# Kernel optimization log

Measured on AMD Instinct MI355X. Metric: run time of the kernel, lower is better.

Reference implementation:

```python
import jax, jax.numpy as jnp
import numpy as np

N, C, HD, E, T, HS, WS = 8, 256, 8, 64, 16, 14, 14
S = HS * WS
EPS = 1e-5
FACTOR = 1.0 / np.sqrt(S * E).astype(np.float32)


def hswish(x):
    return x * jnp.clip(x + 3.0, 0.0, 6.0) * (1.0 / 6.0)


def _bn(x, g, b, m, v):
    shp = (1, -1, 1, 1, 1)
    scale = g / jnp.sqrt(v + EPS)
    return (x - m.reshape(shp)) * scale.reshape(shp) + b.reshape(shp)


def _dwconv(x, w):
    # depthwise Conv3d kernel (1,3,3), padding (0,1,1), groups=C
    return jax.lax.conv_general_dilated(
        x, w, window_strides=(1, 1, 1),
        padding=((0, 0), (1, 1), (1, 1)),
        dimension_numbers=('NCDHW', 'OIDHW', 'NCDHW'),
        feature_group_count=x.shape[1])


def _project(x, dw, g1, b1, m1, v1, pw, pb=None, bn2=None):
    h = hswish(_bn(_dwconv(x, dw), g1, b1, m1, v1))
    y = jnp.einsum('ncthw,oc->nothw', h, pw)
    if pb is not None:
        y = y + pb.reshape(1, -1, 1, 1, 1)
    if bn2 is not None:
        y = _bn(y, *bn2)
    return y


def setup_inputs() -> dict:
    key = jax.random.key(0)
    ks = jax.random.split(key, 8)
    d = {}
    d['x'] = jax.random.normal(ks[0], (N, C, T, HS, WS), jnp.float32)
    for name, k, out in (('theta', ks[1], HD * E), ('phi', ks[2], HD * E), ('g', ks[3], HD * C)):
        k1, k2 = jax.random.split(k)
        d[name + '_dw'] = jax.random.normal(k1, (C, 1, 1, 3, 3), jnp.float32) * 0.2
        d[name + '_bn1_g'] = jnp.ones((C,), jnp.float32)
        d[name + '_bn1_b'] = jnp.zeros((C,), jnp.float32)
        d[name + '_bn1_m'] = jnp.zeros((C,), jnp.float32)
        d[name + '_bn1_v'] = jnp.ones((C,), jnp.float32)
        d[name + '_pw'] = jax.random.normal(k2, (out, C), jnp.float32) * (1.0 / np.sqrt(C).astype(np.float32))
    d['theta_pb'] = jnp.zeros((HD * E,), jnp.float32)
    d['phi_pb'] = jnp.zeros((HD * E,), jnp.float32)
    d['g_bn2_g'] = jnp.ones((HD * C,), jnp.float32)
    d['g_bn2_b'] = jnp.zeros((HD * C,), jnp.float32)
    d['g_bn2_m'] = jnp.zeros((HD * C,), jnp.float32)
    d['g_bn2_v'] = jnp.ones((HD * C,), jnp.float32)
    d['heads_w'] = jax.random.normal(ks[4], (HD, HD), jnp.float32)
    return d


def reference(x, theta_dw, theta_bn1_g, theta_bn1_b, theta_bn1_m, theta_bn1_v, theta_pw, theta_pb,
              phi_dw, phi_bn1_g, phi_bn1_b, phi_bn1_m, phi_bn1_v, phi_pw, phi_pb,
              g_dw, g_bn1_g, g_bn1_b, g_bn1_m, g_bn1_v, g_pw,
              g_bn2_g, g_bn2_b, g_bn2_m, g_bn2_v, heads_w):
    th = _project(x, theta_dw, theta_bn1_g, theta_bn1_b, theta_bn1_m, theta_bn1_v, theta_pw, pb=theta_pb)
    ph = _project(x, phi_dw, phi_bn1_g, phi_bn1_b, phi_bn1_m, phi_bn1_v, phi_pw, pb=phi_pb)
    gg = hswish(_project(x, g_dw, g_bn1_g, g_bn1_b, g_bn1_m, g_bn1_v, g_pw,
                         bn2=(g_bn2_g, g_bn2_b, g_bn2_m, g_bn2_v)))
    TH = th.reshape(N, HD, E, T, S)   # theta features
    PH = ph.reshape(N, HD, E, T, S)   # phi features
    G5 = gg.reshape(N, HD, C, T, S)   # value features
    # adjacency over temporal nodes: [N,H,T,T]
    adj = jax.nn.softmax(FACTOR * jnp.einsum('nhets,nheus->nhtu', TH, PH), axis=-1)
    # GCN step: [N,H,T,C,S]
    gcn = hswish(jnp.einsum('nhtu,nhcus->nhtcs', adj, G5))
    # head-mix attention: [N,T,H]
    hf = gcn.mean(axis=(3, 4)).transpose(0, 2, 1)
    attn = jax.nn.softmax(hf @ heads_w, axis=-1)
    # combine heads: [N,C,T,S] -> [N,C,T,Hs,Ws]
    z = jnp.einsum('nhtcs,nth->ncts', gcn, attn).reshape(N, C, T, HS, WS)
    return hswish(x + z)
```

## Files before the change

### kernel.cpp

```cpp
#include <hip/hip_runtime.h>
#include <hip/hip_bf16.h>

typedef __hip_bfloat16 bf16;
typedef __attribute__((ext_vector_type(4))) float f32x4;
typedef __attribute__((ext_vector_type(8))) short s16x8;

#define DEV static __device__ __forceinline__

namespace {

constexpr float kEPS = 1e-5f;
constexpr float kFACTOR = 1.0f / 112.0f;

DEV float hswish_f(float v) { return v * fminf(fmaxf(v + 3.f, 0.f), 6.f) * (1.f / 6.f); }

DEV void gload_lds16(const bf16* g, bf16* l) {
  __builtin_amdgcn_global_load_lds(
      (const __attribute__((address_space(1))) unsigned int*)g,
      (__attribute__((address_space(3))) unsigned int*)l, 16, 0, 0);
}

__global__ void cvt_pw_kernel(const float* __restrict__ a,
                              const float* __restrict__ b,
                              const float* __restrict__ cG,
                              const float* __restrict__ g2g, const float* __restrict__ g2b,
                              const float* __restrict__ g2m, const float* __restrict__ g2v,
                              bf16* __restrict__ oa, bf16* __restrict__ ob,
                              bf16* __restrict__ oc, float* __restrict__ bnscl,
                              float* __restrict__ bnsft) {
  int i = blockIdx.x * 256 + threadIdx.x;
  if (i < 512 * 256) {
    oa[i] = __float2bfloat16(a[i]);
    ob[i] = __float2bfloat16(b[i]);
  }
  if (i < 2048 * 256) {
    int r = i >> 8, k = i & 255;
    int h = r >> 8, c = r & 255;
    oc[(c * 8 + h) * 256 + k] = __float2bfloat16(cG[i]);
  }
  if (i < 2048) {
    int c = i >> 3, h = i & 7, ref = h * 256 + c;
    float s = g2g[ref] * rsqrtf(g2v[ref] + kEPS);
    bnscl[i] = s;
    bnsft[i] = g2b[ref] - g2m[ref] * s;
  }
}

__global__ __launch_bounds__(256) void conv_kernel(
    const float* __restrict__ x,
    const float* __restrict__ tdw, const float* __restrict__ tg,
    const float* __restrict__ tb, const float* __restrict__ tm, const float* __restrict__ tv,
    const float* __restrict__ pdw, const float* __restrict__ pg,
    const float* __restrict__ pb, const float* __restrict__ pm, const float* __restrict__ pv,
    const float* __restrict__ gdw, const float* __restrict__ gG,
    const float* __restrict__ gb, const float* __restrict__ gm, const float* __restrict__ gv,
    bf16* __restrict__ h_t, bf16* __restrict__ h_p, bf16* __restrict__ h_g) {
  int bid = blockIdx.x;
  int cb = bid & 3, t = (bid >> 2) & 15, n = bid >> 6;
  int c0 = cb * 64;
  __shared__ float xs[64][197];
  __shared__ float wts[3][64][9];
  __shared__ float sc[3][64], sh[3][64];
  int tid = threadIdx.x;
  for (int i = tid; i < 64 * 9; i += 256) {
    int cl = i / 9, k = i % 9;
    wts[0][cl][k] = tdw[(c0 + cl) * 9 + k];
    wts[1][cl][k] = pdw[(c0 + cl) * 9 + k];
    wts[2][cl][k] = gdw[(c0 + cl) * 9 + k];
  }
  if (tid < 64) {
    int c = c0 + tid;
    float s0 = tg[c] * rsqrtf(tv[c] + kEPS);
    sc[0][tid] = s0; sh[0][tid] = tb[c] - tm[c] * s0;
    float s1 = pg[c] * rsqrtf(pv[c] + kEPS);
    sc[1][tid] = s1; sh[1][tid] = pb[c] - pm[c] * s1;
    float s2 = gG[c] * rsqrtf(gv[c] + kEPS);
    sc[2][tid] = s2; sh[2][tid] = gb[c] - gm[c] * s2;
  }
  const float* xb = x + ((size_t)(n * 256 + c0) * 16 + t) * 196;
  for (int i = tid; i < 64 * 196; i += 256) {
    int cl = i / 196, s = i % 196;
    xs[cl][s] = xb[(size_t)cl * 3136 + s];
  }
  __syncthreads();
  for (int i = tid; i < 64 * 196; i += 256) {
    int cl = i & 63, sp = i >> 6;
    int hs = sp / 14, wsp = sp % 14;
    float a0 = 0.f, a1 = 0.f, a2 = 0.f;
    #pragma unroll
    for (int dy = -1; dy <= 1; ++dy) {
      int yy = hs + dy;
      if (yy < 0 || yy >= 14) continue;
      #pragma unroll
      for (int dx = -1; dx <= 1; ++dx) {
        int xx = wsp + dx;
        if (xx < 0 || xx >= 14) continue;
        float v = xs[cl][yy * 14 + xx];
        int k = (dy + 1) * 3 + (dx + 1);
        a0 = fmaf(wts[0][cl][k], v, a0);
        a1 = fmaf(wts[1][cl][k], v, a1);
        a2 = fmaf(wts[2][cl][k], v, a2);
      }
    }
    a0 = hswish_f(a0 * sc[0][cl] + sh[0][cl]);
    a1 = hswish_f(a1 * sc[1][cl] + sh[1][cl]);
    a2 = hswish_f(a2 * sc[2][cl] + sh[2][cl]);
    size_t oidx = ((size_t)n * 3136 + t * 196 + sp) * 256 + c0 + cl;
    h_t[oidx] = __float2bfloat16(a0);
    h_p[oidx] = __float2bfloat16(a1);
    h_g[oidx] = __float2bfloat16(a2);
  }
}

__global__ __launch_bounds__(256) void gemm_op_kernel(
    const bf16* __restrict__ A,
    const bf16* __restrict__ B,
    bf16* __restrict__ D,
    const float* __restrict__ bias) {
  int mt = blockIdx.x, nt = blockIdx.y, n = blockIdx.z;
  __shared__ __align__(16) bf16 lds_a[128 * 64];
  __shared__ __align__(16) bf16 lds_b[64 * 64];
  int tid = threadIdx.x;
  int wid = tid >> 6, lane = tid & 63;
  int wr = wid >> 1, wc = wid & 1;
  int l15 = lane & 15, lh = lane >> 4;
  f32x4 acc[4][2];
  #pragma unroll
  for (int m = 0; m < 4; ++m)
    #pragma unroll
    for (int q = 0; q < 2; ++q) acc[m][q] = (f32x4){0.f, 0.f, 0.f, 0.f};
  const bf16* Ab = A + (size_t)mt * 128 * 256;
  const bf16* Bb = B + ((size_t)n * 3136 + (size_t)nt * 64) * 256;
  for (int k0 = 0; k0 < 256; k0 += 64) {
    #pragma unroll
    for (int it = 0; it < 4; ++it) {
      int g = tid + it * 256;
      int row = g >> 3, c16 = g & 7;
      int4 v = *(const int4*)(Ab + (size_t)row * 256 + k0 + c16 * 8);
      *(int4*)((char*)lds_a + row * 128 + ((c16 * 16) ^ ((row & 7) << 4))) = v;
    }
    #pragma unroll
    for (int it = 0; it < 2; ++it) {
      int g = tid + it * 256;
      int row = g >> 3, c16 = g & 7;
      int4 v = *(const int4*)(Bb + (size_t)row * 256 + k0 + c16 * 8);
      *(int4*)((char*)lds_b + row * 128 + ((c16 * 16) ^ ((row & 7) << 4))) = v;
    }
    __syncthreads();
    #pragma unroll
    for (int kk = 0; kk < 64; kk += 32) {
      s16x8 af[4], bfr[2];
      #pragma unroll
      for (int m = 0; m < 4; ++m) {
        int row = wr * 64 + m * 16 + l15;
        af[m] = *(const s16x8*)((const char*)lds_a + row * 128 +
                                (((kk + lh * 8) * 2) ^ ((row & 7) << 4)));
      }
      #pragma unroll
      for (int q = 0; q < 2; ++q) {
        int row = wc * 32 + q * 16 + l15;
        bfr[q] = *(const s16x8*)((const char*)lds_b + row * 128 +
                                 (((kk + lh * 8) * 2) ^ ((row & 7) << 4)));
      }
      #pragma unroll
      for (int m = 0; m < 4; ++m)
        #pragma unroll
        for (int q = 0; q < 2; ++q)
          acc[m][q] = __builtin_amdgcn_mfma_f32_16x16x32_bf16(af[m], bfr[q], acc[m][q], 0, 0, 0);
    }
    __syncthreads();
  }
  #pragma unroll
  for (int m = 0; m < 4; ++m) {
    #pragma unroll
    for (int q = 0; q < 2; ++q) {
      int col = wc * 32 + q * 16 + l15;
      #pragma unroll
      for (int r = 0; r < 4; ++r) {
        int row = wr * 64 + m * 16 + lh * 4 + r;
        float v = acc[m][q][r] + bias[mt * 128 + row];
        *(bf16*)((char*)lds_a + row * 128 + ((col * 2) ^ ((row & 7) << 4))) =
            __float2bfloat16(v);
      }
    }
  }
  __syncthreads();
  #pragma unroll
  for (int it = 0; it < 4; ++it) {
    int g = tid + it * 256;
    int row = g >> 3, cq = g & 7;
    int4 v = *(const int4*)((const char*)lds_a + row * 128 + ((cq * 16) ^ ((row & 7) << 4)));
    *(int4*)(D + ((size_t)n * 512 + mt * 128 + row) * 3136 + nt * 64 + cq * 8) = v;
  }
}

__global__ __launch_bounds__(256) void gemm_g_kernel(
    const bf16* __restrict__ A,
    const bf16* __restrict__ W,
    bf16* __restrict__ D,
    const float* __restrict__ bnscl, const float* __restrict__ bnsft) {
  int bid = blockIdx.x;
  int n = bid & 7, rem = bid >> 3;
  int otb = rem / 49, tsb = rem % 49;
  __shared__ __align__(16) bf16 lds_a[64 * 64];
  __shared__ __align__(16) bf16 lds_b[256 * 64];
  int tid = threadIdx.x;
  int wid = tid >> 6, lane = tid & 63;
  int l15 = lane & 15, lh = lane >> 4;
  f32x4 acc[4][4];
  #pragma unroll
  for (int m = 0; m < 4; ++m)
    #pragma unroll
    for (int q = 0; q < 4; ++q) acc[m][q] = (f32x4){0.f, 0.f, 0.f, 0.f};
  const bf16* Ab = A + ((size_t)n * 3136 + (size_t)tsb * 64) * 256;
  const bf16* Wb = W + (size_t)otb * 256 * 256;
  int arow = tid >> 3, ac16 = tid & 7;
  for (int k0 = 0; k0 < 256; k0 += 64) {
    #pragma unroll
    for (int it = 0; it < 2; ++it) {
      int row = arow + it * 32;
      gload_lds16(Ab + (size_t)row * 256 + k0 + ((ac16 ^ (row & 7)) * 8),
                  lds_a + (size_t)(row * 8 + ac16) * 8);
    }
    #pragma unroll
    for (int it = 0; it < 8; ++it) {
      int row = arow + it * 32;
      gload_lds16(Wb + (size_t)row * 256 + k0 + ((ac16 ^ (row & 7)) * 8),
                  lds_b + (size_t)(row * 8 + ac16) * 8);
    }
    __syncthreads();
    #pragma unroll
    for (int kk = 0; kk < 64; kk += 32) {
      s16x8 af[4], bfr[4];
      #pragma unroll
      for (int m = 0; m < 4; ++m) {
        int row = m * 16 + l15;
        af[m] = *(const s16x8*)((const char*)lds_a + row * 128 +
                                (((kk + lh * 8) * 2) ^ ((row & 7) << 4)));
      }
      #pragma unroll
      for (int q = 0; q < 4; ++q) {
        int row = wid * 64 + q * 16 + l15;
        bfr[q] = *(const s16x8*)((const char*)lds_b + row * 128 +
                                 (((kk + lh * 8) * 2) ^ ((row & 7) << 4)));
      }
      #pragma unroll
      for (int m = 0; m < 4; ++m)
        #pragma unroll
        for (int q = 0; q < 4; ++q)
          acc[m][q] = __builtin_amdgcn_mfma_f32_16x16x32_bf16(af[m], bfr[q], acc[m][q], 0, 0, 0);
    }
    __syncthreads();
  }
  #pragma unroll
  for (int q = 0; q < 4; ++q) {
    int ocol = wid * 64 + q * 16 + l15;
    float scl = bnscl[otb * 256 + ocol], sft = bnsft[otb * 256 + ocol];
    #pragma unroll
    for (int m = 0; m < 4; ++m) {
      #pragma unroll
      for (int r = 0; r < 4; ++r) {
        int row = m * 16 + lh * 4 + r;
        float v = hswish_f(acc[m][q][r] * scl + sft);
        *(bf16*)((char*)lds_b + row * 512 + ((ocol * 2) ^ ((row & 7) << 4))) =
            __float2bfloat16(v);
      }
    }
  }
  __syncthreads();
  #pragma unroll
  for (int it = 0; it < 8; ++it) {
    int g = tid + it * 256;
    int row = g >> 5, cq = g & 31;
    int4 v = *(const int4*)((const char*)lds_b + row * 512 + ((cq * 16) ^ ((row & 7) << 4)));
    *(int4*)(D + ((size_t)n * 3136 + tsb * 64 + row) * 2048 + otb * 256 + cq * 8) = v;
  }
}

__global__ __launch_bounds__(256) void adj_accum_kernel(const bf16* __restrict__ th,
                                                        const bf16* __restrict__ ph,
                                                        float* __restrict__ adj_raw) {
  int bid = blockIdx.x;
  int eb = bid & 7, h = (bid >> 3) & 7, n = bid >> 6;
  __shared__ __align__(16) float As[16 * 196];
  __shared__ __align__(16) float Bs[16 * 196];
  int tid = threadIdx.x;
  int t = tid >> 4, u = tid & 15;
  float acc = 0.f;
  for (int e8 = 0; e8 < 8; ++e8) {
    int e = eb * 8 + e8;
    const bf16* tp = th + ((size_t)n * 512 + h * 64 + e) * 3136;
    const bf16* pp = ph + ((size_t)n * 512 + h * 64 + e) * 3136;
    __syncthreads();
    for (int i = tid; i < 3136; i += 256) {
      As[i] = __bfloat162float(tp[i]);
      Bs[i] = __bfloat162float(pp[i]);
    }
    __syncthreads();
    const float* ar = As + t * 196;
    const float* br = Bs + u * 196;
    #pragma unroll
    for (int j = 0; j < 49; ++j) {
      f32x4 a = *(const f32x4*)(ar + j * 4);
      f32x4 b = *(const f32x4*)(br + j * 4);
      acc = fmaf(a[0], b[0], acc); acc = fmaf(a[1], b[1], acc);
      acc = fmaf(a[2], b[2], acc); acc = fmaf(a[3], b[3], acc);
    }
  }
  atomicAdd(&adj_raw[((n * 8 + h) * 16 + t) * 16 + u], acc);
}

__global__ void adj_softmax_kernel(const float* __restrict__ raw, float* __restrict__ adj) {
  int r = blockIdx.x * 256 + threadIdx.x;
  if (r >= 1024) return;
  const float* p = raw + r * 16;
  float* q = adj + r * 16;
  float v[16], mx = -1e30f;
  #pragma unroll
  for (int u = 0; u < 16; ++u) { v[u] = p[u] * kFACTOR; mx = fmaxf(mx, v[u]); }
  float s = 0.f;
  #pragma unroll
  for (int u = 0; u < 16; ++u) { v[u] = __expf(v[u] - mx); s += v[u]; }
  float inv = 1.f / s;
  #pragma unroll
  for (int u = 0; u < 16; ++u) q[u] = v[u] * inv;
}

template <int EPI>
__global__ __launch_bounds__(256) void consume_kernel(
    const bf16* __restrict__ gg, const float* __restrict__ adj,
    const float* __restrict__ attn, float* __restrict__ hf,
    bf16* __restrict__ ztmp) {
  int s = blockIdx.x, oh = blockIdx.y, n = blockIdx.z;
  __shared__ __align__(16) float adjL[8][260];
  __shared__ __align__(16) char aux[4096];
  bf16(*zL)[128] = (bf16(*)[128])aux;
  float(*hfp)[8][16] = (float(*)[8][16])aux;
  int tid = threadIdx.x;
  int h = tid & 7;
  for (int i = tid; i < 2048; i += 256) adjL[i >> 8][i & 255] = adj[n * 2048 + i];
  float atn[16];
  if (EPI == 1) {
    #pragma unroll
    for (int t = 0; t < 16; ++t) atn[t] = attn[n * 128 + t * 8 + h];
  }
  __syncthreads();
  const bf16* gbase = gg + ((size_t)n * 3136 + s) * 2048 + oh * 1024 + tid;
  float hacc[16];
  if (EPI == 0) {
    #pragma unroll
    for (int t = 0; t < 16; ++t) hacc[t] = 0.f;
  }
  #pragma unroll
  for (int tb = 0; tb < 4; ++tb) {
    f32x4 aj[4][4];
    #pragma unroll
    for (int tt = 0; tt < 4; ++tt)
      #pragma unroll
      for (int u4 = 0; u4 < 4; ++u4)
        aj[tt][u4] = *(const f32x4*)&adjL[h][(tb * 4 + tt) * 16 + u4 * 4];
    #pragma unroll
    for (int k = 0; k < 4; ++k) {
      const bf16* gp = gbase + k * 256;
      float gv[16];
      #pragma unroll
      for (int u = 0; u < 16; ++u)
        gv[u] = __bfloat162float(gp[(size_t)u * (196 * 2048)]);
      float zp[4];
      #pragma unroll
      for (int tt = 0; tt < 4; ++tt) {
        float z = 0.f;
        #pragma unroll
        for (int u4 = 0; u4 < 4; ++u4) {
          z = fmaf(aj[tt][u4][0], gv[u4 * 4 + 0], z);
          z = fmaf(aj[tt][u4][1], gv[u4 * 4 + 1], z);
          z = fmaf(aj[tt][u4][2], gv[u4 * 4 + 2], z);
          z = fmaf(aj[tt][u4][3], gv[u4 * 4 + 3], z);
        }
        if (EPI == 0) hacc[tb * 4 + tt] += hswish_f(z);
        else zp[tt] = atn[tb * 4 + tt] * hswish_f(z);
      }
      if (EPI == 1) {
        #pragma unroll
        for (int tt = 0; tt < 4; ++tt) {
          zp[tt] += __shfl_xor(zp[tt], 1);
          zp[tt] += __shfl_xor(zp[tt], 2);
          zp[tt] += __shfl_xor(zp[tt], 4);
        }
        if (h < 4)
          zL[tb * 4 + h][(tid >> 3) + k * 32] = __float2bfloat16(zp[h]);
      }
    }
  }
  if (EPI == 0) {
    #pragma unroll
    for (int t = 0; t < 16; ++t) {
      hacc[t] += __shfl_xor(hacc[t], 8);
      hacc[t] += __shfl_xor(hacc[t], 16);
      hacc[t] += __shfl_xor(hacc[t], 32);
    }
    if ((tid & 63) < 8) {
      #pragma unroll
      for (int t = 0; t < 16; ++t) hfp[tid >> 6][h][t] = hacc[t];
    }
    __syncthreads();
    if (tid < 128) {
      int h2 = tid & 7, t2 = tid >> 3;
      float v = hfp[0][h2][t2] + hfp[1][h2][t2] + hfp[2][h2][t2] + hfp[3][h2][t2];
      atomicAdd(&hf[n * 128 + t2 * 8 + h2], v);
    }
  } else {
    __syncthreads();
    int t = tid >> 4, cq = tid & 15;
    int4 v = *(const int4*)&zL[t][cq * 8];
    *(int4*)(ztmp + ((size_t)n * 3136 + t * 196 + s) * 256 + oh * 128 + cq * 8) = v;
  }
}

__global__ void attn_kernel(const float* __restrict__ hf, const float* __restrict__ hw,
                            float* __restrict__ attn) {
  int tid = threadIdx.x;
  if (tid >= 128) return;
  int n = tid >> 4, t = tid & 15;
  const float inv = 1.0f / (256.0f * 196.0f);
  float hm[8];
  #pragma unroll
  for (int h = 0; h < 8; ++h) hm[h] = hf[(n * 16 + t) * 8 + h] * inv;
  float o[8], mx = -1e30f;
  #pragma unroll
  for (int h2 = 0; h2 < 8; ++h2) {
    float s = 0.f;
    #pragma unroll
    for (int h = 0; h < 8; ++h) s = fmaf(hm[h], hw[h * 8 + h2], s);
    o[h2] = s; mx = fmaxf(mx, s);
  }
  float s = 0.f;
  #pragma unroll
  for (int h2 = 0; h2 < 8; ++h2) { o[h2] = __expf(o[h2] - mx); s += o[h2]; }
  float is = 1.f / s;
  #pragma unroll
  for (int h2 = 0; h2 < 8; ++h2) attn[(n * 16 + t) * 8 + h2] = o[h2] * is;
}

__global__ __launch_bounds__(256) void zres_kernel(const bf16* __restrict__ ztmp,
                                                   const float* __restrict__ x,
                                                   float* __restrict__ out) {
  int tsb = blockIdx.x, cb = blockIdx.y, n = blockIdx.z;
  __shared__ __align__(16) bf16 tile[64 * 64];
  int tid = threadIdx.x;
  #pragma unroll
  for (int it = 0; it < 2; ++it) {
    int g = tid + it * 256;
    int row = g >> 3, cq = g & 7;
    int4 v = *(const int4*)(ztmp + ((size_t)n * 3136 + tsb * 64 + row) * 256 + cb * 64 + cq * 8);
    *(int4*)((char*)tile + row * 128 + ((cq * 16) ^ ((row & 7) << 4))) = v;
  }
  __syncthreads();
  int cl = tid & 63, tq = tid >> 6;
  size_t obase = ((size_t)(n * 256 + cb * 64 + cl)) * 3136 + tsb * 64 + tq * 16;
  #pragma unroll
  for (int i = 0; i < 16; i += 4) {
    f32x4 xv = *(const f32x4*)(x + obase + i);
    f32x4 r;
    #pragma unroll
    for (int j = 0; j < 4; ++j) {
      int row = tq * 16 + i + j;
      unsigned short zb = *(const unsigned short*)((const char*)tile + row * 128 +
                                                   ((cl * 2) ^ ((row & 7) << 4)));
      float z = __uint_as_float((unsigned)zb << 16);
      r[j] = hswish_f(xv[j] + z);
    }
    *(f32x4*)(out + obase + i) = r;
  }
}

}

extern "C" void kernel_launch(void* const* d_in, const int* in_sizes, int n_in,
                              void* d_out, int out_size, void* d_ws, size_t ws_size,
                              hipStream_t stream) {
  const float* x       = (const float*)d_in[0];
  const float* t_dw    = (const float*)d_in[1];
  const float* t_g     = (const float*)d_in[2];
  const float* t_b     = (const float*)d_in[3];
  const float* t_m     = (const float*)d_in[4];
  const float* t_v     = (const float*)d_in[5];
  const float* t_pw    = (const float*)d_in[6];
  const float* p_dw    = (const float*)d_in[7];
  const float* p_g     = (const float*)d_in[8];
  const float* p_b     = (const float*)d_in[9];
  const float* p_m     = (const float*)d_in[10];
  const float* p_v     = (const float*)d_in[11];
  const float* p_pw    = (const float*)d_in[12];
  const float* g_dw    = (const float*)d_in[13];
  const float* g_g     = (const float*)d_in[14];
  const float* g_b     = (const float*)d_in[15];
  const float* g_m     = (const float*)d_in[16];
  const float* g_v     = (const float*)d_in[17];
  const float* g_pw    = (const float*)d_in[18];
  const float* t_pb    = (const float*)d_in[19];
  const float* p_pb    = (const float*)d_in[20];
  const float* g2_g    = (const float*)d_in[21];
  const float* g2_b    = (const float*)d_in[22];
  const float* g2_m    = (const float*)d_in[23];
  const float* g2_v    = (const float*)d_in[24];
  const float* heads_w = (const float*)d_in[25];
  float* out = (float*)d_out;
  (void)in_sizes; (void)n_in; (void)out_size; (void)ws_size;

  char* w = (char*)d_ws;
  size_t off = 0;
  auto take = [&](size_t bytes) {
    char* p = w + off;
    off = (off + bytes + 255) & ~(size_t)255;
    return p;
  };
  bf16* pwT = (bf16*)take(512 * 256 * 2);
  bf16* pwP = (bf16*)take(512 * 256 * 2);
  bf16* pwG = (bf16*)take(2048 * 256 * 2);
  float* bnscl = (float*)take(2048 * 4);
  float* bnsft = (float*)take(2048 * 4);
  bf16* hT  = (bf16*)take((size_t)8 * 3136 * 256 * 2);
  bf16* hP  = (bf16*)take((size_t)8 * 3136 * 256 * 2);
  bf16* hG  = (bf16*)take((size_t)8 * 3136 * 256 * 2);
  bf16* th  = (bf16*)take((size_t)8 * 512 * 3136 * 2);
  bf16* ph  = (bf16*)take((size_t)8 * 512 * 3136 * 2);
  bf16* gg  = (bf16*)take((size_t)8 * 3136 * 2048 * 2);
  float* adj_raw = (float*)take(1024 * 16 * 4);
  float* adj     = (float*)take(1024 * 16 * 4);
  float* hf      = (float*)take(1024 * 4);
  float* attn    = (float*)take(1024 * 4);
  bf16* ztmp = hT;

  hipMemsetAsync(adj_raw, 0, 1024 * 16 * 4, stream);
  hipMemsetAsync(hf, 0, 1024 * 4, stream);

  cvt_pw_kernel<<<2048, 256, 0, stream>>>(t_pw, p_pw, g_pw, g2_g, g2_b, g2_m, g2_v,
                                          pwT, pwP, pwG, bnscl, bnsft);
  conv_kernel<<<512, 256, 0, stream>>>(x, t_dw, t_g, t_b, t_m, t_v,
                                       p_dw, p_g, p_b, p_m, p_v,
                                       g_dw, g_g, g_b, g_m, g_v, hT, hP, hG);
  gemm_op_kernel<<<dim3(4, 49, 8), 256, 0, stream>>>(pwT, hT, th, t_pb);
  gemm_op_kernel<<<dim3(4, 49, 8), 256, 0, stream>>>(pwP, hP, ph, p_pb);
  gemm_g_kernel<<<3136, 256, 0, stream>>>(hG, pwG, gg, bnscl, bnsft);
  adj_accum_kernel<<<512, 256, 0, stream>>>(th, ph, adj_raw);
  adj_softmax_kernel<<<4, 256, 0, stream>>>(adj_raw, adj);
  consume_kernel<0><<<dim3(196, 2, 8), 256, 0, stream>>>(gg, adj, nullptr, hf, nullptr);
  attn_kernel<<<1, 128, 0, stream>>>(hf, heads_w, attn);
  consume_kernel<1><<<dim3(196, 2, 8), 256, 0, stream>>>(gg, adj, attn, nullptr, ztmp);
  zres_kernel<<<dim3(49, 4, 8), 256, 0, stream>>>(ztmp, x, out);
}
```

Measured before the change: 432.1 us.

## Store g-projection with time innermost so consumer loads 16 timesteps vectorized

The g-projection GEMM now gathers A rows so each 64-row tile covers 4 spatial positions across all 16 timesteps, and writes its output as [n][s][channel][t] with t contiguous. The consume kernel then reads the 16 temporal values per channel with two 16-byte loads instead of 16 strided 2-byte loads, unpacking bf16 via bit shifts. This targets uncoalesced, strided global loads in the consumer. In exchange, the GEMM epilogue's LDS transpose writes are now unswizzled scalar stores, which may cause bank conflicts.

New measurement: 415.8 us. 3.8% less time.

```diff
diff --git a/kernel.cpp b/kernel.cpp
--- a/kernel.cpp
+++ b/kernel.cpp
@@ -13,6 +13,8 @@
 constexpr float kFACTOR = 1.0f / 112.0f;
 
 DEV float hswish_f(float v) { return v * fminf(fmaxf(v + 3.f, 0.f), 6.f) * (1.f / 6.f); }
+DEV float blo(unsigned r) { return __uint_as_float(r << 16); }
+DEV float bhi(unsigned r) { return __uint_as_float(r & 0xFFFF0000u); }
 
 DEV void gload_lds16(const bf16* g, bf16* l) {
   __builtin_amdgcn_global_load_lds(
@@ -201,7 +203,7 @@
     const float* __restrict__ bnscl, const float* __restrict__ bnsft) {
   int bid = blockIdx.x;
   int n = bid & 7, rem = bid >> 3;
-  int otb = rem / 49, tsb = rem % 49;
+  int otb = rem / 49, sb = rem % 49;
   __shared__ __align__(16) bf16 lds_a[64 * 64];
   __shared__ __align__(16) bf16 lds_b[256 * 64];
   int tid = threadIdx.x;
@@ -212,14 +214,15 @@
   for (int m = 0; m < 4; ++m)
     #pragma unroll
     for (int q = 0; q < 4; ++q) acc[m][q] = (f32x4){0.f, 0.f, 0.f, 0.f};
-  const bf16* Ab = A + ((size_t)n * 3136 + (size_t)tsb * 64) * 256;
+  const bf16* Ab = A + (size_t)n * 3136 * 256;
   const bf16* Wb = W + (size_t)otb * 256 * 256;
   int arow = tid >> 3, ac16 = tid & 7;
   for (int k0 = 0; k0 < 256; k0 += 64) {
     #pragma unroll
     for (int it = 0; it < 2; ++it) {
       int row = arow + it * 32;
-      gload_lds16(Ab + (size_t)row * 256 + k0 + ((ac16 ^ (row & 7)) * 8),
+      int ts = (row >> 2) * 196 + sb * 4 + (row & 3);
+      gload_lds16(Ab + (size_t)ts * 256 + k0 + ((ac16 ^ (row & 7)) * 8),
                   lds_a + (size_t)(row * 8 + ac16) * 8);
     }
     #pragma unroll
@@ -261,9 +264,9 @@
       #pragma unroll
       for (int r = 0; r < 4; ++r) {
         int row = m * 16 + lh * 4 + r;
+        int u = row >> 2, si = row & 3;
         float v = hswish_f(acc[m][q][r] * scl + sft);
-        *(bf16*)((char*)lds_b + row * 512 + ((ocol * 2) ^ ((row & 7) << 4))) =
-            __float2bfloat16(v);
+        lds_b[(si * 256 + ocol) * 16 + u] = __float2bfloat16(v);
       }
     }
   }
@@ -271,9 +274,10 @@
   #pragma unroll
   for (int it = 0; it < 8; ++it) {
     int g = tid + it * 256;
-    int row = g >> 5, cq = g & 31;
-    int4 v = *(const int4*)((const char*)lds_b + row * 512 + ((cq * 16) ^ ((row & 7) << 4)));
-    *(int4*)(D + ((size_t)n * 3136 + tsb * 64 + row) * 2048 + otb * 256 + cq * 8) = v;
+    int si = g >> 9, remg = g & 511;
+    size_t dst = ((size_t)n * 196 + sb * 4 + si) * (2048 * 16) +
+                 (size_t)otb * 256 * 16 + (size_t)remg * 8;
+    *(int4*)(D + dst) = *(const int4*)(lds_b + (size_t)g * 8);
   }
 }
 
@@ -345,7 +349,8 @@
     for (int t = 0; t < 16; ++t) atn[t] = attn[n * 128 + t * 8 + h];
   }
   __syncthreads();
-  const bf16* gbase = gg + ((size_t)n * 3136 + s) * 2048 + oh * 1024 + tid;
+  const bf16* gbase = gg + (size_t)n * (3136 * 2048) + (size_t)s * (2048 * 16) +
+                      (size_t)(oh * 1024 + tid) * 16;
   float hacc[16];
   if (EPI == 0) {
     #pragma unroll
@@ -361,11 +366,14 @@
         aj[tt][u4] = *(const f32x4*)&adjL[h][(tb * 4 + tt) * 16 + u4 * 4];
     #pragma unroll
     for (int k = 0; k < 4; ++k) {
-      const bf16* gp = gbase + k * 256;
+      const bf16* gp = gbase + (size_t)k * (256 * 16);
+      uint4 ra = *(const uint4*)gp;
+      uint4 rb = *(const uint4*)(gp + 8);
       float gv[16];
-      #pragma unroll
-      for (int u = 0; u < 16; ++u)
-        gv[u] = __bfloat162float(gp[(size_t)u * (196 * 2048)]);
+      gv[0] = blo(ra.x); gv[1] = bhi(ra.x); gv[2] = blo(ra.y); gv[3] = bhi(ra.y);
+      gv[4] = blo(ra.z); gv[5] = bhi(ra.z); gv[6] = blo(ra.w); gv[7] = bhi(ra.w);
+      gv[8] = blo(rb.x); gv[9] = bhi(rb.x); gv[10] = blo(rb.y); gv[11] = bhi(rb.y);
+      gv[12] = blo(rb.z); gv[13] = bhi(rb.z); gv[14] = blo(rb.w); gv[15] = bhi(rb.w);
       float zp[4];
       #pragma unroll
       for (int tt = 0; tt < 4; ++tt) {
```
